# Kernel optimization log

Measured on AMD Instinct MI355X. Metric: run time of the kernel, lower is better.

## Reference

```python
import jax, jax.numpy as jnp
import numpy as np
import math

E = 256; H = 8; MLP = 1024; LAT = 128; TOPK = 32
IH = 4; IDH = 8  # LightningIndexer: num_heads=4, indexer_head_dim=8
B, R, C = 2, 1024, 4


def setup_inputs() -> dict:
    key = jax.random.key(0)
    ks = jax.random.split(key, 12)
    s = 0.02
    def nrm(k, shape, scale=s):
        return jax.random.normal(k, shape, jnp.float32) * scale
    return {
        "src": jax.random.normal(ks[0], (B, R, C, E), jnp.float32),
        "train_test_split_index": 768,
        "fa_in_w": nrm(ks[1], (3 * E, E)), "fa_in_b": jnp.zeros((3 * E,), jnp.float32),
        "fa_out_w": nrm(ks[2], (E, E)), "fa_out_b": jnp.zeros((E,), jnp.float32),
        "norm1_g": jnp.ones((E,), jnp.float32), "norm1_b": jnp.zeros((E,), jnp.float32),
        "idx_q_w": nrm(ks[3], (IH * IDH, E)), "idx_k_w": nrm(ks[4], (IH * IDH, E)),
        "idx_out_w": jax.random.normal(ks[5], (IH,), jnp.float32),
        "mla_q_w": nrm(ks[6], (E, E)), "mla_down_w": nrm(ks[7], (LAT, E)),
        "mla_up_w": nrm(ks[8], (2 * E, LAT)), "mla_out_w": nrm(ks[9], (E, E)),
        "norm2_g": jnp.ones((E,), jnp.float32), "norm2_b": jnp.zeros((E,), jnp.float32),
        "lin1_w": nrm(ks[10], (MLP, E)), "lin1_b": jnp.zeros((MLP,), jnp.float32),
        "lin2_w": nrm(ks[11], (E, MLP)), "lin2_b": jnp.zeros((E,), jnp.float32),
        "norm3_g": jnp.ones((E,), jnp.float32), "norm3_b": jnp.zeros((E,), jnp.float32),
    }


def _ln(x, g, b, eps=1e-5):
    m = x.mean(-1, keepdims=True)
    v = ((x - m) ** 2).mean(-1, keepdims=True)
    return (x - m) * jax.lax.rsqrt(v + eps) * g + b


def _mha(x, in_w, in_b, out_w, out_b):
    # torch nn.MultiheadAttention, batch_first, self-attention
    Bf, S, D = x.shape
    dh = D // H
    qkv = x @ in_w.T + in_b
    q, k, v = jnp.split(qkv, 3, axis=-1)
    q = q.reshape(Bf, S, H, dh); k = k.reshape(Bf, S, H, dh); v = v.reshape(Bf, S, H, dh)
    a = jnp.einsum('bqhd,bkhd->bhqk', q, k) / math.sqrt(dh)
    a = jax.nn.softmax(a, axis=-1)
    o = jnp.einsum('bhqk,bkhd->bqhd', a, v).reshape(Bf, S, D)
    return o @ out_w.T + out_b


def _indexer(xq, xk, qw, kw, ow, top_k):
    # int8-quantized scoring: matmul -> scale -> relu -> head-weighted sum -> topk
    Bf, NQ, _ = xq.shape
    NK = xk.shape[1]
    q = (xq @ qw.T).reshape(Bf, NQ, IH, IDH).transpose(0, 2, 1, 3)  # [B,IH,NQ,IDH]
    k = (xk @ kw.T).reshape(Bf, NK, IH, IDH).transpose(0, 2, 1, 3)
    qs = (jnp.abs(q).max(axis=(2, 3), keepdims=True) + 1e-6) / 127.0
    ks_ = (jnp.abs(k).max(axis=(2, 3), keepdims=True) + 1e-6) / 127.0
    qi = jnp.clip(jnp.round(q / qs), -127, 127)
    ki = jnp.clip(jnp.round(k / ks_), -127, 127)
    scores = jax.nn.relu(jnp.einsum('bhqd,bhkd->bhqk', qi, ki) * (qs * ks_))
    red = jnp.einsum('bhqk,h->bqk', scores, ow)
    _, idx = jax.lax.top_k(red, top_k)
    return idx  # [B, NQ, top_k]


def _mla_sparse(xq, xkv, idx, qw, dw, uw, ow):
    # gather per-query top-k compressed latents, up-project, attend
    Bf, NQ, D = xq.shape
    dh = D // H
    K = idx.shape[2]
    q = (xq @ qw.T).reshape(Bf, NQ, H, dh)
    c = xkv @ dw.T                                    # [B, NKV, LAT]
    c_sel = c[jnp.arange(Bf)[:, None, None], idx]     # [B, NQ, K, LAT]
    kv = (c_sel @ uw.T).reshape(Bf, NQ, K, 2, H, dh)
    k, v = kv[..., 0, :, :], kv[..., 1, :, :]
    score = (q[:, :, None, :, :] * k).sum(-1) / math.sqrt(dh)  # [B,NQ,K,H]
    w = jax.nn.softmax(score, axis=2)
    out = (w[..., None] * v).sum(axis=2).reshape(Bf, NQ, D)
    return out @ ow.T


def reference(src, train_test_split_index, fa_in_w, fa_in_b, fa_out_w, fa_out_b,
              norm1_g, norm1_b, idx_q_w, idx_k_w, idx_out_w,
              mla_q_w, mla_down_w, mla_up_w, mla_out_w,
              norm2_g, norm2_b, lin1_w, lin1_b, lin2_w, lin2_b, norm3_g, norm3_b):
    Bz, Rz, Cz, D = src.shape
    split = int(train_test_split_index)
    # feature attention across columns
    sf = src.reshape(Bz * Rz, Cz, D)
    sf = _mha(sf, fa_in_w, fa_in_b, fa_out_w, fa_out_b) + sf
    src = _ln(sf.reshape(Bz, Rz, Cz, D), norm1_g, norm1_b)
    # row attention with DSA sparse top-k selection
    st = src.transpose(0, 2, 1, 3).reshape(Bz * Cz, Rz, D)
    x_tr, x_te = st[:, :split], st[:, split:]
    k_sel = min(TOPK, split)
    tr_idx = _indexer(x_tr, x_tr, idx_q_w, idx_k_w, idx_out_w, k_sel)
    tr_out = _mla_sparse(x_tr, x_tr, tr_idx, mla_q_w, mla_down_w, mla_up_w, mla_out_w)
    te_idx = _indexer(x_te, x_tr, idx_q_w, idx_k_w, idx_out_w, k_sel)
    te_out = _mla_sparse(x_te, x_tr, te_idx, mla_q_w, mla_down_w, mla_up_w, mla_out_w)
    st = st + jnp.concatenate([tr_out, te_out], axis=1)
    src = st.reshape(Bz, Cz, Rz, D).transpose(0, 2, 1, 3)
    src = _ln(src, norm2_g, norm2_b)
    h = jax.nn.gelu(src @ lin1_w.T + lin1_b, approximate=False)
    src = h @ lin2_w.T + lin2_b + src
    return _ln(src, norm3_g, norm3_b)
```

## Files before the change

### kernel.cpp

```cpp
#include <hip/hip_runtime.h>
#include <hip/hip_bf16.h>
#include <cmath>

#define E_ 256
#define H_ 8
#define DH 32
#define MLPD 1024
#define LATD 128
#define TOPK_ 32
#define BB 2
#define RR 1024
#define CC 4
#define NT 8192
#define BF 8
#define SPLIT 768

using bf16x8 = __attribute__((ext_vector_type(8))) short;
using f32x4v = __attribute__((ext_vector_type(4))) float;

__device__ __forceinline__ unsigned short f2b(float x) {
    __hip_bfloat16 h = __float2bfloat16(x);
    return *reinterpret_cast<unsigned short*>(&h);
}
__device__ __forceinline__ float b2f(unsigned short u) {
    return __uint_as_float(((unsigned)u) << 16);
}

struct ConvArgs {
    const float* s[10];
    unsigned short* d[10];
    int cum[10];
};
__global__ __launch_bounds__(256) void convert_f2b(ConvArgs a, int totq)
{
    int q = blockIdx.x * 256 + threadIdx.x;
    if (q >= totq) return;
    int seg = 0;
    while (q >= a.cum[seg]) seg++;
    int lq = q - (seg ? a.cum[seg - 1] : 0);
    float4 v = ((const float4*)a.s[seg])[lq];
    ushort4 o;
    o.x = f2b(v.x); o.y = f2b(v.y); o.z = f2b(v.z); o.w = f2b(v.w);
    ((ushort4*)a.d[seg])[lq] = o;
}

template<int TM, int TN, int BIAS, int GELU, int RES, int AMAP, int OMAP, int OUTBF>
__global__ __launch_bounds__(256) void gemm_mfma(
    const unsigned short* __restrict__ A, const unsigned short* __restrict__ W,
    const float* __restrict__ bias, const float* __restrict__ res,
    float* __restrict__ Cf, unsigned short* __restrict__ Ch,
    int M, int N, int K)
{
    __shared__ __align__(16) unsigned short As[TM * 40];
    __shared__ __align__(16) unsigned short Bs[TN * 40];
    const int tid = threadIdx.x;
    const int lane = tid & 63, wave = tid >> 6;
    const int wr = wave >> 1, wc = wave & 1;
    const int m0 = blockIdx.y * TM, n0 = blockIdx.x * TN;

    int ra, kqa;
    if constexpr (TM == 128) { ra = tid >> 1; kqa = (tid & 1) * 16; }
    else                     { ra = tid >> 2; kqa = (tid & 3) * 8; }
    int rb, kqb;
    if constexpr (TN == 128) { rb = tid >> 1; kqb = (tid & 1) * 16; }
    else                     { rb = tid >> 2; kqb = (tid & 3) * 8; }

    int am = m0 + ra;
    size_t arow = AMAP ? ((size_t)(am / SPLIT) * RR + (am % SPLIT)) : (size_t)am;
    const unsigned short* Ap = A + arow * (size_t)K + kqa;
    const unsigned short* Bp = W + (size_t)(n0 + rb) * K + kqb;

    constexpr int FM = TM / 32, FN = TN / 32;
    f32x4v acc[FM][FN];
#pragma unroll
    for (int i = 0; i < FM; i++)
#pragma unroll
        for (int j = 0; j < FN; j++) acc[i][j] = (f32x4v){0.f, 0.f, 0.f, 0.f};

    const int kof = (lane >> 4) * 8;
    int arow_lds[FM], brow_lds[FN];
#pragma unroll
    for (int f = 0; f < FM; f++)
        arow_lds[f] = (wr * (TM / 2) + f * 16 + (lane & 15)) * 40 + kof;
#pragma unroll
    for (int f = 0; f < FN; f++)
        brow_lds[f] = (wc * (TN / 2) + f * 16 + (lane & 15)) * 40 + kof;

    for (int k0 = 0; k0 < K; k0 += 32) {
        int4 va0, va1, vb0, vb1;
        va0 = *(const int4*)(Ap + k0);
        if constexpr (TM == 128) va1 = *(const int4*)(Ap + k0 + 8);
        vb0 = *(const int4*)(Bp + k0);
        if constexpr (TN == 128) vb1 = *(const int4*)(Bp + k0 + 8);
        __syncthreads();
        *(int4*)&As[ra * 40 + kqa] = va0;
        if constexpr (TM == 128) *(int4*)&As[ra * 40 + kqa + 8] = va1;
        *(int4*)&Bs[rb * 40 + kqb] = vb0;
        if constexpr (TN == 128) *(int4*)&Bs[rb * 40 + kqb + 8] = vb1;
        __syncthreads();
        bf16x8 af[FM], bfr[FN];
#pragma unroll
        for (int f = 0; f < FM; f++) af[f] = *(const bf16x8*)&As[arow_lds[f]];
#pragma unroll
        for (int f = 0; f < FN; f++) bfr[f] = *(const bf16x8*)&Bs[brow_lds[f]];
#pragma unroll
        for (int fm = 0; fm < FM; fm++)
#pragma unroll
            for (int fn = 0; fn < FN; fn++)
                acc[fm][fn] = __builtin_amdgcn_mfma_f32_16x16x32_bf16(
                    af[fm], bfr[fn], acc[fm][fn], 0, 0, 0);
    }

#pragma unroll
    for (int fm = 0; fm < FM; fm++) {
#pragma unroll
        for (int r = 0; r < 4; r++) {
            int row = m0 + wr * (TM / 2) + fm * 16 + ((lane >> 4) << 2) + r;
            size_t orow;
            if (OMAP) {
                int bc = row >> 10, rr = row & 1023;
                int b = bc >> 2, c = bc & 3;
                orow = ((size_t)(b * RR + rr)) * CC + c;
            } else orow = (size_t)row;
#pragma unroll
            for (int fn = 0; fn < FN; fn++) {
                int col = n0 + wc * (TN / 2) + fn * 16 + (lane & 15);
                float v = acc[fm][fn][r];
                if (BIAS) v += bias[col];
                if (GELU) v = 0.5f * v * (1.0f + erff(v * 0.70710678118654752f));
                if (RES)  v += res[(size_t)row * N + col];
                if (OUTBF) Ch[orow * (size_t)N + col] = f2b(v);
                else       Cf[orow * (size_t)N + col] = v;
            }
        }
    }
}

__global__ __launch_bounds__(256) void fa_attn(const float* __restrict__ qkv,
                                               unsigned short* __restrict__ outb)
{
    int seq = blockIdx.x, tid = threadIdx.x;
    __shared__ float sq[4][E_], sk[4][E_], sv[4][E_];
    __shared__ float ss[H_][4][4];
    __shared__ float sw[H_][4][4];
    const float4* base = (const float4*)(qkv + (size_t)seq * 3072);
#pragma unroll
    for (int p = 0; p < 3; p++) {
        int pos = tid + p * 256;
        float4 v = base[pos];
        int i = pos / 192, c4 = pos % 192;
        if (c4 < 64)       *(float4*)&sq[i][c4 * 4] = v;
        else if (c4 < 128) *(float4*)&sk[i][(c4 - 64) * 4] = v;
        else               *(float4*)&sv[i][(c4 - 128) * 4] = v;
    }
    __syncthreads();
    if (tid < 128) {
        int h = tid >> 4, i = (tid >> 2) & 3, j = tid & 3;
        float s = 0;
        for (int d = 0; d < DH; d++) s += sq[i][h * DH + d] * sk[j][h * DH + d];
        ss[h][i][j] = s * 0.17677669529663688f;
    }
    __syncthreads();
    if (tid < 32) {
        int h = tid >> 2, i = tid & 3;
        float m = ss[h][i][0];
        for (int j = 1; j < 4; j++) m = fmaxf(m, ss[h][i][j]);
        float e[4], sum = 0;
        for (int j = 0; j < 4; j++) { e[j] = expf(ss[h][i][j] - m); sum += e[j]; }
        float inv = 1.0f / sum;
        for (int j = 0; j < 4; j++) sw[h][i][j] = e[j] * inv;
    }
    __syncthreads();
    int e = tid, h = e >> 5;
    for (int i = 0; i < 4; i++) {
        float o = 0;
        for (int j = 0; j < 4; j++) o += sw[h][i][j] * sv[j][e];
        outb[((size_t)(seq * 4 + i)) * E_ + e] = f2b(o);
    }
}

template<int OMAP, int WB>
__global__ __launch_bounds__(256) void ln_k(const float* __restrict__ in,
                                            const float* __restrict__ g,
                                            const float* __restrict__ bta,
                                            float* __restrict__ out,
                                            unsigned short* __restrict__ outh)
{
    int row = blockIdx.x * 4 + (threadIdx.x >> 6);
    int t = threadIdx.x & 63;
    float4 v = ((const float4*)(in + (size_t)row * E_))[t];
    float s = v.x + v.y + v.z + v.w;
#pragma unroll
    for (int o = 32; o >= 1; o >>= 1) s += __shfl_xor(s, o);
    float mean = s * (1.0f / E_);
    float dx0 = v.x - mean, dx1 = v.y - mean, dx2 = v.z - mean, dx3 = v.w - mean;
    float q = dx0 * dx0 + dx1 * dx1 + dx2 * dx2 + dx3 * dx3;
#pragma unroll
    for (int o = 32; o >= 1; o >>= 1) q += __shfl_xor(q, o);
    float inv = rsqrtf(q * (1.0f / E_) + 1e-5f);
    size_t orow;
    if (OMAP == 1) {
        int b = row >> 12, r = (row >> 2) & 1023, c = row & 3;
        orow = ((size_t)(b * CC + c)) * RR + r;
    } else orow = (size_t)row;
    int c0 = t * 4;
    float4 o;
    o.x = dx0 * inv * g[c0 + 0] + bta[c0 + 0];
    o.y = dx1 * inv * g[c0 + 1] + bta[c0 + 1];
    o.z = dx2 * inv * g[c0 + 2] + bta[c0 + 2];
    o.w = dx3 * inv * g[c0 + 3] + bta[c0 + 3];
    ((float4*)(out + orow * E_))[t] = o;
    if (WB) {
        ushort4 oh; oh.x = f2b(o.x); oh.y = f2b(o.y); oh.z = f2b(o.z); oh.w = f2b(o.w);
        ((ushort4*)(outh + orow * E_))[t] = oh;
    }
}

__global__ __launch_bounds__(256) void idx_scales(const float* __restrict__ qk32,
                                                  float* __restrict__ scl)
{
    int id = blockIdx.x;
    int type = id / 32, bf = (id % 32) >> 2, h = id & 3;
    int cofs = (type == 2) ? 32 : 0;
    int r0 = (type == 1) ? SPLIT : 0;
    int r1 = (type == 1) ? RR : SPLIT;
    float m = 0;
    for (int r = r0 + (int)threadIdx.x; r < r1; r += 256) {
        const float* p = qk32 + ((size_t)(bf * RR + r)) * 64 + cofs + h * 8;
        for (int dd = 0; dd < 8; dd++) m = fmaxf(m, fabsf(p[dd]));
    }
#pragma unroll
    for (int o = 32; o >= 1; o >>= 1) m = fmaxf(m, __shfl_xor(m, o));
    __shared__ float red[4];
    if ((threadIdx.x & 63) == 0) red[threadIdx.x >> 6] = m;
    __syncthreads();
    if (threadIdx.x == 0) {
        m = fmaxf(fmaxf(red[0], red[1]), fmaxf(red[2], red[3]));
        scl[id] = (m + 1e-6f) / 127.0f;
    }
}

__global__ __launch_bounds__(256) void idx_quantk(const float* __restrict__ qk32,
                                                  const float* __restrict__ scl,
                                                  signed char* __restrict__ ki8)
{
    int gi = blockIdx.x * 256 + threadIdx.x;
    int bf = gi / (SPLIT * 32);
    int rem = gi % (SPLIT * 32);
    int r = rem >> 5, d = rem & 31, h = d >> 3;
    float ks = scl[64 + bf * 4 + h];
    float v = qk32[((size_t)(bf * RR + r)) * 64 + 32 + d];
    float qq = fminf(fmaxf(rintf(v / ks), -127.f), 127.f);
    ki8[gi] = (signed char)qq;
}

__global__ __launch_bounds__(256) void idx_score_topk(const float* __restrict__ qk32,
                                                      const signed char* __restrict__ ki8,
                                                      const float* __restrict__ scl,
                                                      const float* __restrict__ ow,
                                                      int* __restrict__ idx_out)
{
    int bid = blockIdx.x, tid = threadIdx.x;
    int bf = bid >> 10, qr = bid & 1023;
    int sel = (qr < SPLIT) ? 0 : 32;
    __shared__ float qi[32];
    __shared__ float fac[4];
    __shared__ unsigned keyhi[SPLIT];
    __shared__ __align__(16) unsigned long long cand[SPLIT];
    __shared__ int hist[256], hist2[256], Sarr[256];
    __shared__ int bsel1, bsel2, ccnt;

    hist[tid] = 0; hist2[tid] = 0;
    if (tid == 0) ccnt = 0;
    if (tid < 32) {
        int h = tid >> 3;
        float qs = scl[sel + bf * 4 + h];
        float v = qk32[(size_t)bid * 64 + tid];
        qi[tid] = fminf(fmaxf(rintf(v / qs), -127.f), 127.f);
    }
    if (tid < 4) {
        float qs = scl[sel + bf * 4 + tid];
        float ks = scl[64 + bf * 4 + tid];
        fac[tid] = __fmul_rn(qs, ks);
    }
    __syncthreads();
    float ow0 = ow[0], ow1 = ow[1], ow2 = ow[2], ow3 = ow[3];
    for (int k = tid; k < SPLIT; k += 256) {
        const int4* kp4 = (const int4*)(ki8 + ((size_t)(bf * SPLIT + k)) * 32);
        int4 w0 = kp4[0], w1 = kp4[1];
        int wd[8] = {w0.x, w0.y, w0.z, w0.w, w1.x, w1.y, w1.z, w1.w};
        float owv[4] = {ow0, ow1, ow2, ow3};
        float r = 0;
#pragma unroll
        for (int h = 0; h < 4; h++) {
            float dot = 0.f;
#pragma unroll
            for (int b = 0; b < 2; b++) {
                unsigned int w = (unsigned int)wd[h * 2 + b];
#pragma unroll
                for (int by = 0; by < 4; by++) {
                    float kv = (float)((signed char)(w >> (8 * by)));
                    dot = fmaf(qi[h * 8 + b * 4 + by], kv, dot);
                }
            }
            float sc = fmaxf(__fmul_rn(dot, fac[h]), 0.f);
            r = __fadd_rn(r, __fmul_rn(sc, owv[h]));
        }
        unsigned int bitsv = __float_as_uint(r);
        unsigned int mono = (bitsv & 0x80000000u) ? ~bitsv : (bitsv | 0x80000000u);
        if (mono == 0x7FFFFFFFu) mono = 0x80000000u;
        keyhi[k] = mono;
        atomicAdd(&hist[mono >> 24], 1);
    }
    __syncthreads();
    if (tid < 64) {
        int4 h4 = *(const int4*)&hist[tid * 4];
        int local = h4.x + h4.y + h4.z + h4.w;
        int s = local;
#pragma unroll
        for (int o = 1; o < 64; o <<= 1) {
            int x = __shfl_down(s, o);
            if (tid + o < 64) s += x;
        }
        int sufE = s - local;
        Sarr[tid * 4 + 0] = sufE + h4.y + h4.z + h4.w;
        Sarr[tid * 4 + 1] = sufE + h4.z + h4.w;
        Sarr[tid * 4 + 2] = sufE + h4.w;
        Sarr[tid * 4 + 3] = sufE;
    }
    __syncthreads();
    if (Sarr[tid] < TOPK_ && Sarr[tid] + hist[tid] >= TOPK_) bsel1 = tid;
    __syncthreads();
    const int b1 = bsel1;
    const int S1 = Sarr[b1];
    for (int k = tid; k < SPLIT; k += 256) {
        unsigned mono = keyhi[k];
        if ((int)(mono >> 24) == b1) atomicAdd(&hist2[(mono >> 16) & 255], 1);
    }
    __syncthreads();
    if (tid < 64) {
        int4 h4 = *(const int4*)&hist2[tid * 4];
        int local = h4.x + h4.y + h4.z + h4.w;
        int s = local;
#pragma unroll
        for (int o = 1; o < 64; o <<= 1) {
            int x = __shfl_down(s, o);
            if (tid + o < 64) s += x;
        }
        int sufE = s - local;
        Sarr[tid * 4 + 0] = sufE + h4.y + h4.z + h4.w;
        Sarr[tid * 4 + 1] = sufE + h4.z + h4.w;
        Sarr[tid * 4 + 2] = sufE + h4.w;
        Sarr[tid * 4 + 3] = sufE;
    }
    __syncthreads();
    if (S1 + Sarr[tid] < TOPK_ && S1 + Sarr[tid] + hist2[tid] >= TOPK_) bsel2 = tid;
    __syncthreads();
    const int b2 = bsel2;
    for (int k = tid; k < SPLIT; k += 256) {
        unsigned mono = keyhi[k];
        int hi = mono >> 24, mid = (mono >> 16) & 255;
        if (hi > b1 || (hi == b1 && mid >= b2)) {
            int s = atomicAdd(&ccnt, 1);
            cand[s] = ((unsigned long long)mono << 10) | (unsigned)(1023 - k);
        }
    }
    __syncthreads();
    const int n = ccnt;
    for (int ci = tid; ci < n; ci += 256) {
        unsigned long long mine = cand[ci];
        int r = 0;
        for (int j = 0; j < n; j++) r += (cand[j] > mine);
        if (r < TOPK_)
            idx_out[(size_t)bid * TOPK_ + r] = 1023 - (int)(mine & 1023ull);
    }
}

__global__ __launch_bounds__(256) void mla_g(const float* __restrict__ qb,
                                             const float* __restrict__ uw,
                                             unsigned short* __restrict__ G16)
{
    int qt = blockIdx.x, h = blockIdx.y, tid = threadIdx.x;
    __shared__ float Qs[64][33];
    __shared__ float Us[32][132];
    {
        int r = tid >> 2, c0 = (tid & 3) * 8;
        const float* srcp = qb + ((size_t)(qt * 64 + r)) * E_ + h * DH + c0;
        float4 a = ((const float4*)srcp)[0];
        float4 b = ((const float4*)srcp)[1];
        Qs[r][c0 + 0] = a.x; Qs[r][c0 + 1] = a.y; Qs[r][c0 + 2] = a.z; Qs[r][c0 + 3] = a.w;
        Qs[r][c0 + 4] = b.x; Qs[r][c0 + 5] = b.y; Qs[r][c0 + 6] = b.z; Qs[r][c0 + 7] = b.w;
    }
    {
        int d = tid >> 3, l0 = (tid & 7) * 16;
        const float* srcp = uw + (size_t)(h * DH + d) * LATD + l0;
#pragma unroll
        for (int ii = 0; ii < 4; ii++) {
            float4 v = ((const float4*)srcp)[ii];
            *(float4*)&Us[d][l0 + ii * 4] = v;
        }
    }
    __syncthreads();
    int rg = tid >> 5, l = (tid & 31) * 4;
    float acc[8][4];
#pragma unroll
    for (int i = 0; i < 8; i++)
#pragma unroll
        for (int j = 0; j < 4; j++) acc[i][j] = 0.f;
    for (int d = 0; d < DH; d++) {
        float4 u = *(const float4*)&Us[d][l];
#pragma unroll
        for (int i = 0; i < 8; i++) {
            float qv = Qs[rg * 8 + i][d];
            acc[i][0] += qv * u.x; acc[i][1] += qv * u.y;
            acc[i][2] += qv * u.z; acc[i][3] += qv * u.w;
        }
    }
#pragma unroll
    for (int i = 0; i < 8; i++) {
        ushort4 o;
        o.x = f2b(acc[i][0]); o.y = f2b(acc[i][1]);
        o.z = f2b(acc[i][2]); o.w = f2b(acc[i][3]);
        *(ushort4*)(G16 + ((size_t)(qt * 64 + rg * 8 + i)) * 1024 + h * 128 + l) = o;
    }
}

__global__ __launch_bounds__(64) void mla_attn(const unsigned short* __restrict__ G16,
                                               const unsigned short* __restrict__ cb16,
                                               const int* __restrict__ idxb,
                                               unsigned short* __restrict__ Mo16)
{
    const int bid = blockIdx.x, l = threadIdx.x;
    const int bf = bid >> 10;
    __shared__ __align__(16) unsigned short ct[128][40];
    __shared__ __align__(16) unsigned short wT[16][40];
    __shared__ int sidx[32];
    if (l < 32) sidx[l] = idxb[(size_t)bid * 32 + l];

    const int n16 = l & 15, g = l >> 4;

    {
        int j = l >> 1, c0 = (l & 1) * 64;
        const unsigned short* crow = cb16 + ((size_t)(bf * SPLIT + sidx[j])) * 128 + c0;
#pragma unroll
        for (int e = 0; e < 8; e++) {
            uint4 v = *(const uint4*)(crow + e * 8);
            unsigned short tmp[8];
            *(uint4*)tmp = v;
#pragma unroll
            for (int t = 0; t < 8; t++) ct[c0 + e * 8 + t][j] = tmp[t];
        }
    }

    const unsigned short* Ab = G16 + (size_t)bid * 1024 + (size_t)(l & 7) * 128 + g * 8;
    const int j0 = sidx[n16], j1 = sidx[16 + n16];
    const unsigned short* B0 = cb16 + ((size_t)(bf * SPLIT + j0)) * 128 + g * 8;
    const unsigned short* B1 = cb16 + ((size_t)(bf * SPLIT + j1)) * 128 + g * 8;
    f32x4v s0 = {0.f, 0.f, 0.f, 0.f}, s1 = {0.f, 0.f, 0.f, 0.f};
#pragma unroll
    for (int c = 0; c < 4; c++) {
        bf16x8 a  = *(const bf16x8*)(Ab + c * 32);
        bf16x8 b0 = *(const bf16x8*)(B0 + c * 32);
        bf16x8 b1 = *(const bf16x8*)(B1 + c * 32);
        s0 = __builtin_amdgcn_mfma_f32_16x16x32_bf16(a, b0, s0, 0, 0, 0);
        s1 = __builtin_amdgcn_mfma_f32_16x16x32_bf16(a, b1, s1, 0, 0, 0);
    }

    const float scale = 0.17677669529663688f;
#pragma unroll
    for (int r = 0; r < 4; r++) {
        float a0 = s0[r] * scale, a1 = s1[r] * scale;
        float mx = fmaxf(a0, a1);
#pragma unroll
        for (int o = 1; o < 16; o <<= 1) mx = fmaxf(mx, __shfl_xor(mx, o));
        float e0 = expf(a0 - mx), e1 = expf(a1 - mx);
        float sm = e0 + e1;
#pragma unroll
        for (int o = 1; o < 16; o <<= 1) sm += __shfl_xor(sm, o);
        float inv = 1.0f / sm;
        wT[g * 4 + r][n16]      = f2b(e0 * inv);
        wT[g * 4 + r][16 + n16] = f2b(e1 * inv);
    }

    bf16x8 aw = *(const bf16x8*)&wT[n16][g * 8];
#pragma unroll
    for (int t = 0; t < 8; t++) {
        bf16x8 bc = *(const bf16x8*)&ct[t * 16 + n16][g * 8];
        f32x4v m = {0.f, 0.f, 0.f, 0.f};
        m = __builtin_amdgcn_mfma_f32_16x16x32_bf16(aw, bc, m, 0, 0, 0);
        if (g < 2) {
#pragma unroll
            for (int r = 0; r < 4; r++)
                Mo16[(size_t)bid * 1024 + (size_t)(g * 4 + r) * 128 + t * 16 + n16] = f2b(m[r]);
        }
    }
}

__global__ __launch_bounds__(256) void mla_out(const unsigned short* __restrict__ Mo16,
                                               const float* __restrict__ uw,
                                               unsigned short* __restrict__ ob)
{
    int qt = blockIdx.x, h = blockIdx.y, tid = threadIdx.x;
    __shared__ float Ms[64][132];
    __shared__ float Us[32][129];
    {
        int r = tid >> 2, l0 = (tid & 3) * 32;
        const unsigned short* srcp = Mo16 + ((size_t)(qt * 64 + r)) * 1024 + h * 128 + l0;
#pragma unroll
        for (int ii = 0; ii < 4; ii++) {
            uint4 v = ((const uint4*)srcp)[ii];
            unsigned short u[8];
            *(uint4*)u = v;
#pragma unroll
            for (int t = 0; t < 8; t++) Ms[r][l0 + ii * 8 + t] = b2f(u[t]);
        }
    }
    {
        int d = tid >> 3, l0 = (tid & 7) * 16;
        const float* srcp = uw + (size_t)(256 + h * DH + d) * LATD + l0;
#pragma unroll
        for (int ii = 0; ii < 4; ii++) {
            float4 v = ((const float4*)srcp)[ii];
            Us[d][l0 + ii * 4 + 0] = v.x; Us[d][l0 + ii * 4 + 1] = v.y;
            Us[d][l0 + ii * 4 + 2] = v.z; Us[d][l0 + ii * 4 + 3] = v.w;
        }
    }
    __syncthreads();
    int d = tid & 31, rg = tid >> 5;
    float acc[8] = {0, 0, 0, 0, 0, 0, 0, 0};
    for (int ll = 0; ll < 128; ll++) {
        float u = Us[d][ll];
#pragma unroll
        for (int i = 0; i < 8; i++) acc[i] += Ms[rg * 8 + i][ll] * u;
    }
#pragma unroll
    for (int i = 0; i < 8; i++)
        ob[((size_t)(qt * 64 + rg * 8 + i)) * E_ + h * DH + d] = f2b(acc[i]);
}

extern "C" void kernel_launch(void* const* d_in, const int* in_sizes, int n_in,
                              void* d_out, int out_size, void* d_ws, size_t ws_size,
                              hipStream_t stream)
{
    (void)in_sizes; (void)n_in; (void)out_size; (void)ws_size;
    const float* src      = (const float*)d_in[0];
    const float* fa_in_w  = (const float*)d_in[2];
    const float* fa_in_b  = (const float*)d_in[3];
    const float* fa_out_w = (const float*)d_in[4];
    const float* fa_out_b = (const float*)d_in[5];
    const float* n1g = (const float*)d_in[6];
    const float* n1b = (const float*)d_in[7];
    const float* iqw = (const float*)d_in[8];
    const float* ikw = (const float*)d_in[9];
    const float* iow = (const float*)d_in[10];
    const float* mqw = (const float*)d_in[11];
    const float* mdw = (const float*)d_in[12];
    const float* muw = (const float*)d_in[13];
    const float* mow = (const float*)d_in[14];
    const float* n2g = (const float*)d_in[15];
    const float* n2b = (const float*)d_in[16];
    const float* l1w = (const float*)d_in[17];
    const float* l1b = (const float*)d_in[18];
    const float* l2w = (const float*)d_in[19];
    const float* l2b = (const float*)d_in[20];
    const float* n3g = (const float*)d_in[21];
    const float* n3b = (const float*)d_in[22];

    float* ws = (float*)d_ws;
    size_t off = 0;
    auto alloc = [&](size_t n) { float* p = ws + off; off += (n + 3) & ~(size_t)3; return p; };

    float* bigA = alloc((size_t)NT * 1024);
    float* Mh   = alloc((size_t)NT * 1024);
    float* tbuf = alloc((size_t)NT * E_);
    float* stb  = alloc((size_t)NT * E_);
    float* cbws = alloc((size_t)BF * SPLIT * LATD / 2 + 16);
    unsigned short* actBF1 = (unsigned short*)alloc((size_t)NT * E_ / 2);
    unsigned short* actBF2 = (unsigned short*)alloc((size_t)NT * E_ / 2);
    float* qk32 = alloc((size_t)NT * 64);
    float* scl = alloc(128);
    int*   idxb = (int*)alloc((size_t)NT * 32);
    signed char* ki8 = (signed char*)alloc((size_t)NT * 32 / 4);
    unsigned short* w16 = (unsigned short*)alloc(950272 / 2 + 8);
    unsigned short* wqk16 = (unsigned short*)alloc(16384 / 2 + 8);

    unsigned short* fa_in_w16  = w16;
    unsigned short* fa_out_w16 = fa_in_w16 + 196608;
    unsigned short* mqw16      = fa_out_w16 + 65536;
    unsigned short* mdw16      = mqw16 + 65536;
    unsigned short* mow16      = mdw16 + 32768;
    unsigned short* l1w16      = mow16 + 65536;
    unsigned short* l2w16      = l1w16 + 262144;

    float* qkv = bigA;
    unsigned short* G16 = (unsigned short*)bigA;
    float* x2  = bigA;
    unsigned short* Mo16 = (unsigned short*)Mh;
    unsigned short* h116 = (unsigned short*)Mh;
    float* qb = tbuf;
    unsigned short* cb16 = (unsigned short*)cbws;
    unsigned short* src16  = actBF1;
    unsigned short* abuf16 = actBF1;
    unsigned short* stb16  = actBF1;
    unsigned short* ob16   = actBF2;
    unsigned short* x216   = actBF2;

    ConvArgs ca;
    const float* segs[10] = {src, fa_in_w, fa_out_w, mqw, mdw, mow, l1w, l2w, iqw, ikw};
    unsigned short* segd[10] = {src16, fa_in_w16, fa_out_w16, mqw16, mdw16, mow16, l1w16, l2w16,
                                wqk16, wqk16 + 8192};
    int segn[10] = {NT * E_, 196608, 65536, 65536, 32768, 65536, 262144, 262144, 8192, 8192};
    int cum = 0;
    for (int i = 0; i < 10; i++) { ca.s[i] = segs[i]; ca.d[i] = segd[i]; cum += segn[i] / 4; ca.cum[i] = cum; }
    int totq = cum;
    convert_f2b<<<(totq + 255) / 256, 256, 0, stream>>>(ca, totq);

    dim3 blk(256);
    gemm_mfma<128,128,1,0,0,0,0,0><<<dim3(6,64), blk, 0, stream>>>(src16, fa_in_w16, fa_in_b, nullptr, qkv, nullptr, NT, 768, 256);
    fa_attn<<<2048, blk, 0, stream>>>(qkv, abuf16);
    gemm_mfma<128,64,1,0,1,0,0,0><<<dim3(4,64), blk, 0, stream>>>(abuf16, fa_out_w16, fa_out_b, src, tbuf, nullptr, NT, 256, 256);
    ln_k<1,1><<<NT/4, blk, 0, stream>>>(tbuf, n1g, n1b, stb, stb16);
    gemm_mfma<128,64,0,0,0,0,0,0><<<dim3(1,64), blk, 0, stream>>>(stb16, wqk16, nullptr, nullptr, qk32, nullptr, NT, 64, 256);
    idx_scales<<<96, blk, 0, stream>>>(qk32, scl);
    idx_quantk<<<(BF * SPLIT * 32) / 256, blk, 0, stream>>>(qk32, scl, ki8);
    idx_score_topk<<<NT, blk, 0, stream>>>(qk32, ki8, scl, iow, idxb);
    gemm_mfma<64,64,0,0,0,1,0,1><<<dim3(2,96), blk, 0, stream>>>(stb16, mdw16, nullptr, nullptr, nullptr, cb16, BF * SPLIT, 128, 256);
    gemm_mfma<128,64,0,0,0,0,0,0><<<dim3(4,64), blk, 0, stream>>>(stb16, mqw16, nullptr, nullptr, qb, nullptr, NT, 256, 256);
    mla_g<<<dim3(128,8), blk, 0, stream>>>(qb, muw, G16);
    mla_attn<<<NT, dim3(64), 0, stream>>>(G16, cb16, idxb, Mo16);
    mla_out<<<dim3(128,8), blk, 0, stream>>>(Mo16, muw, ob16);
    gemm_mfma<128,64,0,0,1,0,1,0><<<dim3(4,64), blk, 0, stream>>>(ob16, mow16, nullptr, stb, tbuf, nullptr, NT, 256, 256);
    ln_k<0,1><<<NT/4, blk, 0, stream>>>(tbuf, n2g, n2b, x2, x216);
    gemm_mfma<128,128,1,1,0,0,0,1><<<dim3(8,64), blk, 0, stream>>>(x216, l1w16, l1b, nullptr, nullptr, h116, NT, MLPD, 256);
    gemm_mfma<128,64,1,0,1,0,0,0><<<dim3(4,64), blk, 0, stream>>>(h116, l2w16, l2b, x2, tbuf, nullptr, NT, 256, MLPD);
    ln_k<0,0><<<NT/4, blk, 0, stream>>>(tbuf, n3g, n3b, (float*)d_out, nullptr);
}
```

Measured before the change: 309.6 us.

## Fold MLA query/up/out projections into precomputed weights and merge indexer kernels

Precomputes W2 = U_k^T·Wq and W3 = Wo·U_v per head in a new weight-prep kernel. This replaces the q-projection GEMM, the mla_g kernel, the mla_out kernel and the output GEMM with two MFMA GEMMs (K=256→N=1024 and K=1024→N=256). The QKV projection now writes bf16 instead of fp32 to halve traffic into fa_attn. idx_scales and idx_quantk are merged into one kernel, and mla_attn packs four queries per 256-thread block. The trade-off is extra rounding from the bf16 products of the folded weights and a per-call weight-fold kernel.

```diff
diff --git a/kernel.cpp b/kernel.cpp
--- a/kernel.cpp
+++ b/kernel.cpp
@@ -27,9 +27,9 @@
 }
 
 struct ConvArgs {
-    const float* s[10];
-    unsigned short* d[10];
-    int cum[10];
+    const float* s[8];
+    unsigned short* d[8];
+    int cum[8];
 };
 __global__ __launch_bounds__(256) void convert_f2b(ConvArgs a, int totq)
 {
@@ -42,6 +42,33 @@
     ushort4 o;
     o.x = f2b(v.x); o.y = f2b(v.y); o.z = f2b(v.z); o.w = f2b(v.w);
     ((ushort4*)a.d[seg])[lq] = o;
+}
+
+__global__ __launch_bounds__(256) void make_w2w3(const float* __restrict__ mqw,
+                                                 const float* __restrict__ muw,
+                                                 const float* __restrict__ mow,
+                                                 unsigned short* __restrict__ W2,
+                                                 unsigned short* __restrict__ W3)
+{
+    int b = blockIdx.x, t = threadIdx.x;
+    if (b < 1024) {
+        int h = b >> 7, l = b & 127;
+        float s2 = 0;
+#pragma unroll 8
+        for (int d = 0; d < 32; d++)
+            s2 += muw[(size_t)(h * 32 + d) * 128 + l] * mqw[(size_t)(h * 32 + d) * 256 + t];
+        W2[(size_t)b * 256 + t] = f2b(s2);
+    } else {
+        int e = b - 1024;
+        for (int tt = t; tt < 1024; tt += 256) {
+            int h = tt >> 7, l = tt & 127;
+            float s3 = 0;
+#pragma unroll 8
+            for (int d = 0; d < 32; d++)
+                s3 += muw[(size_t)(256 + h * 32 + d) * 128 + l] * mow[(size_t)e * 256 + h * 32 + d];
+            W3[(size_t)e * 1024 + tt] = f2b(s3);
+        }
+    }
 }
 
 template<int TM, int TN, int BIAS, int GELU, int RES, int AMAP, int OMAP, int OUTBF>
@@ -136,22 +163,27 @@
     }
 }
 
-__global__ __launch_bounds__(256) void fa_attn(const float* __restrict__ qkv,
+__global__ __launch_bounds__(256) void fa_attn(const unsigned short* __restrict__ qkv16,
                                                unsigned short* __restrict__ outb)
 {
     int seq = blockIdx.x, tid = threadIdx.x;
     __shared__ float sq[4][E_], sk[4][E_], sv[4][E_];
     __shared__ float ss[H_][4][4];
     __shared__ float sw[H_][4][4];
-    const float4* base = (const float4*)(qkv + (size_t)seq * 3072);
-#pragma unroll
-    for (int p = 0; p < 3; p++) {
+    const uint4* base = (const uint4*)(qkv16 + (size_t)seq * 3072);
+#pragma unroll
+    for (int p = 0; p < 2; p++) {
         int pos = tid + p * 256;
-        float4 v = base[pos];
-        int i = pos / 192, c4 = pos % 192;
-        if (c4 < 64)       *(float4*)&sq[i][c4 * 4] = v;
-        else if (c4 < 128) *(float4*)&sk[i][(c4 - 64) * 4] = v;
-        else               *(float4*)&sv[i][(c4 - 128) * 4] = v;
+        if (pos < 384) {
+            uint4 v = base[pos];
+            unsigned short u[8];
+            *(uint4*)u = v;
+            int flat = pos * 8;
+            int i = flat / 768, c = flat % 768;
+            float* dst = (c < 256) ? &sq[i][c] : (c < 512) ? &sk[i][c - 256] : &sv[i][c - 512];
+#pragma unroll
+            for (int t = 0; t < 8; t++) dst[t] = b2f(u[t]);
+        }
     }
     __syncthreads();
     if (tid < 128) {
@@ -216,8 +248,9 @@
     }
 }
 
-__global__ __launch_bounds__(256) void idx_scales(const float* __restrict__ qk32,
-                                                  float* __restrict__ scl)
+__global__ __launch_bounds__(256) void idx_scales_quant(const float* __restrict__ qk32,
+                                                        float* __restrict__ scl,
+                                                        signed char* __restrict__ ki8)
 {
     int id = blockIdx.x;
     int type = id / 32, bf = (id % 32) >> 2, h = id & 3;
@@ -232,26 +265,26 @@
 #pragma unroll
     for (int o = 32; o >= 1; o >>= 1) m = fmaxf(m, __shfl_xor(m, o));
     __shared__ float red[4];
+    __shared__ float sscl;
     if ((threadIdx.x & 63) == 0) red[threadIdx.x >> 6] = m;
     __syncthreads();
     if (threadIdx.x == 0) {
         m = fmaxf(fmaxf(red[0], red[1]), fmaxf(red[2], red[3]));
-        scl[id] = (m + 1e-6f) / 127.0f;
-    }
-}
-
-__global__ __launch_bounds__(256) void idx_quantk(const float* __restrict__ qk32,
-                                                  const float* __restrict__ scl,
-                                                  signed char* __restrict__ ki8)
-{
-    int gi = blockIdx.x * 256 + threadIdx.x;
-    int bf = gi / (SPLIT * 32);
-    int rem = gi % (SPLIT * 32);
-    int r = rem >> 5, d = rem & 31, h = d >> 3;
-    float ks = scl[64 + bf * 4 + h];
-    float v = qk32[((size_t)(bf * RR + r)) * 64 + 32 + d];
-    float qq = fminf(fmaxf(rintf(v / ks), -127.f), 127.f);
-    ki8[gi] = (signed char)qq;
+        float sc = (m + 1e-6f) / 127.0f;
+        scl[id] = sc;
+        sscl = sc;
+    }
+    __syncthreads();
+    if (type == 2) {
+        float ks = sscl;
+        for (int r = threadIdx.x; r < SPLIT; r += 256) {
+            const float* p = qk32 + ((size_t)(bf * RR + r)) * 64 + 32 + h * 8;
+            signed char* o = ki8 + ((size_t)(bf * SPLIT + r)) * 32 + h * 8;
+#pragma unroll
+            for (int dd = 0; dd < 8; dd++)
+                o[dd] = (signed char)fminf(fmaxf(rintf(p[dd] / ks), -127.f), 127.f);
+        }
+    }
 }
 
 __global__ __launch_bounds__(256) void idx_score_topk(const float* __restrict__ qk32,
@@ -376,84 +409,36 @@
     }
 }
 
-__global__ __launch_bounds__(256) void mla_g(const float* __restrict__ qb,
-                                             const float* __restrict__ uw,
-                                             unsigned short* __restrict__ G16)
-{
-    int qt = blockIdx.x, h = blockIdx.y, tid = threadIdx.x;
-    __shared__ float Qs[64][33];
-    __shared__ float Us[32][132];
-    {
-        int r = tid >> 2, c0 = (tid & 3) * 8;
-        const float* srcp = qb + ((size_t)(qt * 64 + r)) * E_ + h * DH + c0;
-        float4 a = ((const float4*)srcp)[0];
-        float4 b = ((const float4*)srcp)[1];
-        Qs[r][c0 + 0] = a.x; Qs[r][c0 + 1] = a.y; Qs[r][c0 + 2] = a.z; Qs[r][c0 + 3] = a.w;
-        Qs[r][c0 + 4] = b.x; Qs[r][c0 + 5] = b.y; Qs[r][c0 + 6] = b.z; Qs[r][c0 + 7] = b.w;
-    }
-    {
-        int d = tid >> 3, l0 = (tid & 7) * 16;
-        const float* srcp = uw + (size_t)(h * DH + d) * LATD + l0;
-#pragma unroll
-        for (int ii = 0; ii < 4; ii++) {
-            float4 v = ((const float4*)srcp)[ii];
-            *(float4*)&Us[d][l0 + ii * 4] = v;
-        }
-    }
-    __syncthreads();
-    int rg = tid >> 5, l = (tid & 31) * 4;
-    float acc[8][4];
-#pragma unroll
-    for (int i = 0; i < 8; i++)
-#pragma unroll
-        for (int j = 0; j < 4; j++) acc[i][j] = 0.f;
-    for (int d = 0; d < DH; d++) {
-        float4 u = *(const float4*)&Us[d][l];
-#pragma unroll
-        for (int i = 0; i < 8; i++) {
-            float qv = Qs[rg * 8 + i][d];
-            acc[i][0] += qv * u.x; acc[i][1] += qv * u.y;
-            acc[i][2] += qv * u.z; acc[i][3] += qv * u.w;
-        }
-    }
-#pragma unroll
-    for (int i = 0; i < 8; i++) {
-        ushort4 o;
-        o.x = f2b(acc[i][0]); o.y = f2b(acc[i][1]);
-        o.z = f2b(acc[i][2]); o.w = f2b(acc[i][3]);
-        *(ushort4*)(G16 + ((size_t)(qt * 64 + rg * 8 + i)) * 1024 + h * 128 + l) = o;
-    }
-}
-
-__global__ __launch_bounds__(64) void mla_attn(const unsigned short* __restrict__ G16,
-                                               const unsigned short* __restrict__ cb16,
-                                               const int* __restrict__ idxb,
-                                               unsigned short* __restrict__ Mo16)
-{
-    const int bid = blockIdx.x, l = threadIdx.x;
+__global__ __launch_bounds__(256) void mla_attn(const unsigned short* __restrict__ G16,
+                                                const unsigned short* __restrict__ cb16,
+                                                const int* __restrict__ idxb,
+                                                unsigned short* __restrict__ Mo16)
+{
+    const int w = threadIdx.x >> 6, l = threadIdx.x & 63;
+    const int bid = blockIdx.x * 4 + w;
     const int bf = bid >> 10;
-    __shared__ __align__(16) unsigned short ct[128][40];
-    __shared__ __align__(16) unsigned short wT[16][40];
-    __shared__ int sidx[32];
-    if (l < 32) sidx[l] = idxb[(size_t)bid * 32 + l];
+    __shared__ __align__(16) unsigned short ct[4][128][40];
+    __shared__ __align__(16) unsigned short wT[4][16][40];
+    __shared__ int sidx[4][32];
+    if (l < 32) sidx[w][l] = idxb[(size_t)bid * 32 + l];
 
     const int n16 = l & 15, g = l >> 4;
 
     {
         int j = l >> 1, c0 = (l & 1) * 64;
-        const unsigned short* crow = cb16 + ((size_t)(bf * SPLIT + sidx[j])) * 128 + c0;
+        const unsigned short* crow = cb16 + ((size_t)(bf * SPLIT + sidx[w][j])) * 128 + c0;
 #pragma unroll
         for (int e = 0; e < 8; e++) {
             uint4 v = *(const uint4*)(crow + e * 8);
             unsigned short tmp[8];
             *(uint4*)tmp = v;
 #pragma unroll
-            for (int t = 0; t < 8; t++) ct[c0 + e * 8 + t][j] = tmp[t];
+            for (int t = 0; t < 8; t++) ct[w][c0 + e * 8 + t][j] = tmp[t];
         }
     }
 
     const unsigned short* Ab = G16 + (size_t)bid * 1024 + (size_t)(l & 7) * 128 + g * 8;
-    const int j0 = sidx[n16], j1 = sidx[16 + n16];
+    const int j0 = sidx[w][n16], j1 = sidx[w][16 + n16];
     const unsigned short* B0 = cb16 + ((size_t)(bf * SPLIT + j0)) * 128 + g * 8;
     const unsigned short* B1 = cb16 + ((size_t)(bf * SPLIT + j1)) * 128 + g * 8;
     f32x4v s0 = {0.f, 0.f, 0.f, 0.f}, s1 = {0.f, 0.f, 0.f, 0.f};
@@ -478,14 +463,14 @@
 #pragma unroll
         for (int o = 1; o < 16; o <<= 1) sm += __shfl_xor(sm, o);
         float inv = 1.0f / sm;
-        wT[g * 4 + r][n16]      = f2b(e0 * inv);
-        wT[g * 4 + r][16 + n16] = f2b(e1 * inv);
-    }
-
-    bf16x8 aw = *(const bf16x8*)&wT[n16][g * 8];
+        wT[w][g * 4 + r][n16]      = f2b(e0 * inv);
+        wT[w][g * 4 + r][16 + n16] = f2b(e1 * inv);
+    }
+
+    bf16x8 aw = *(const bf16x8*)&wT[w][n16][g * 8];
 #pragma unroll
     for (int t = 0; t < 8; t++) {
-        bf16x8 bc = *(const bf16x8*)&ct[t * 16 + n16][g * 8];
+        bf16x8 bc = *(const bf16x8*)&ct[w][t * 16 + n16][g * 8];
         f32x4v m = {0.f, 0.f, 0.f, 0.f};
         m = __builtin_amdgcn_mfma_f32_16x16x32_bf16(aw, bc, m, 0, 0, 0);
         if (g < 2) {
@@ -494,48 +479,6 @@
                 Mo16[(size_t)bid * 1024 + (size_t)(g * 4 + r) * 128 + t * 16 + n16] = f2b(m[r]);
         }
     }
-}
-
-__global__ __launch_bounds__(256) void mla_out(const unsigned short* __restrict__ Mo16,
-                                               const float* __restrict__ uw,
-                                               unsigned short* __restrict__ ob)
-{
-    int qt = blockIdx.x, h = blockIdx.y, tid = threadIdx.x;
-    __shared__ float Ms[64][132];
-    __shared__ float Us[32][129];
-    {
-        int r = tid >> 2, l0 = (tid & 3) * 32;
-        const unsigned short* srcp = Mo16 + ((size_t)(qt * 64 + r)) * 1024 + h * 128 + l0;
-#pragma unroll
-        for (int ii = 0; ii < 4; ii++) {
-            uint4 v = ((const uint4*)srcp)[ii];
-            unsigned short u[8];
-            *(uint4*)u = v;
-#pragma unroll
-            for (int t = 0; t < 8; t++) Ms[r][l0 + ii * 8 + t] = b2f(u[t]);
-        }
-    }
-    {
-        int d = tid >> 3, l0 = (tid & 7) * 16;
-        const float* srcp = uw + (size_t)(256 + h * DH + d) * LATD + l0;
-#pragma unroll
-        for (int ii = 0; ii < 4; ii++) {
-            float4 v = ((const float4*)srcp)[ii];
-            Us[d][l0 + ii * 4 + 0] = v.x; Us[d][l0 + ii * 4 + 1] = v.y;
-            Us[d][l0 + ii * 4 + 2] = v.z; Us[d][l0 + ii * 4 + 3] = v.w;
-        }
-    }
-    __syncthreads();
-    int d = tid & 31, rg = tid >> 5;
-    float acc[8] = {0, 0, 0, 0, 0, 0, 0, 0};
-    for (int ll = 0; ll < 128; ll++) {
-        float u = Us[d][ll];
-#pragma unroll
-        for (int i = 0; i < 8; i++) acc[i] += Ms[rg * 8 + i][ll] * u;
-    }
-#pragma unroll
-    for (int i = 0; i < 8; i++)
-        ob[((size_t)(qt * 64 + rg * 8 + i)) * E_ + h * DH + d] = f2b(acc[i]);
 }
 
 extern "C" void kernel_launch(void* const* d_in, const int* in_sizes, int n_in,
@@ -581,55 +524,51 @@
     float* scl = alloc(128);
     int*   idxb = (int*)alloc((size_t)NT * 32);
     signed char* ki8 = (signed char*)alloc((size_t)NT * 32 / 4);
-    unsigned short* w16 = (unsigned short*)alloc(950272 / 2 + 8);
+    unsigned short* w16 = (unsigned short*)alloc(819200 / 2 + 16);
     unsigned short* wqk16 = (unsigned short*)alloc(16384 / 2 + 8);
+    unsigned short* W2_16 = (unsigned short*)alloc(262144 / 2 + 8);
+    unsigned short* W3_16 = (unsigned short*)alloc(262144 / 2 + 8);
 
     unsigned short* fa_in_w16  = w16;
     unsigned short* fa_out_w16 = fa_in_w16 + 196608;
-    unsigned short* mqw16      = fa_out_w16 + 65536;
-    unsigned short* mdw16      = mqw16 + 65536;
-    unsigned short* mow16      = mdw16 + 32768;
-    unsigned short* l1w16      = mow16 + 65536;
+    unsigned short* mdw16      = fa_out_w16 + 65536;
+    unsigned short* l1w16      = mdw16 + 32768;
     unsigned short* l2w16      = l1w16 + 262144;
 
-    float* qkv = bigA;
+    unsigned short* qkv16 = (unsigned short*)bigA;
     unsigned short* G16 = (unsigned short*)bigA;
     float* x2  = bigA;
     unsigned short* Mo16 = (unsigned short*)Mh;
     unsigned short* h116 = (unsigned short*)Mh;
-    float* qb = tbuf;
     unsigned short* cb16 = (unsigned short*)cbws;
     unsigned short* src16  = actBF1;
     unsigned short* abuf16 = actBF1;
     unsigned short* stb16  = actBF1;
-    unsigned short* ob16   = actBF2;
     unsigned short* x216   = actBF2;
 
     ConvArgs ca;
-    const float* segs[10] = {src, fa_in_w, fa_out_w, mqw, mdw, mow, l1w, l2w, iqw, ikw};
-    unsigned short* segd[10] = {src16, fa_in_w16, fa_out_w16, mqw16, mdw16, mow16, l1w16, l2w16,
-                                wqk16, wqk16 + 8192};
-    int segn[10] = {NT * E_, 196608, 65536, 65536, 32768, 65536, 262144, 262144, 8192, 8192};
+    const float* segs[8] = {src, fa_in_w, fa_out_w, mdw, l1w, l2w, iqw, ikw};
+    unsigned short* segd[8] = {src16, fa_in_w16, fa_out_w16, mdw16, l1w16, l2w16,
+                               wqk16, wqk16 + 8192};
+    int segn[8] = {NT * E_, 196608, 65536, 32768, 262144, 262144, 8192, 8192};
     int cum = 0;
-    for (int i = 0; i < 10; i++) { ca.s[i] = segs[i]; ca.d[i] = segd[i]; cum += segn[i] / 4; ca.cum[i] = cum; }
+    for (int i = 0; i < 8; i++) { ca.s[i] = segs[i]; ca.d[i] = segd[i]; cum += segn[i] / 4; ca.cum[i] = cum; }
     int totq = cum;
     convert_f2b<<<(totq + 255) / 256, 256, 0, stream>>>(ca, totq);
+    make_w2w3<<<1280, 256, 0, stream>>>(mqw, muw, mow, W2_16, W3_16);
 
     dim3 blk(256);
-    gemm_mfma<128,128,1,0,0,0,0,0><<<dim3(6,64), blk, 0, stream>>>(src16, fa_in_w16, fa_in_b, nullptr, qkv, nullptr, NT, 768, 256);
-    fa_attn<<<2048, blk, 0, stream>>>(qkv, abuf16);
+    gemm_mfma<128,128,1,0,0,0,0,1><<<dim3(6,64), blk, 0, stream>>>(src16, fa_in_w16, fa_in_b, nullptr, nullptr, qkv16, NT, 768, 256);
+    fa_attn<<<2048, blk, 0, stream>>>(qkv16, abuf16);
     gemm_mfma<128,64,1,0,1,0,0,0><<<dim3(4,64), blk, 0, stream>>>(abuf16, fa_out_w16, fa_out_b, src, tbuf, nullptr, NT, 256, 256);
     ln_k<1,1><<<NT/4, blk, 0, stream>>>(tbuf, n1g, n1b, stb, stb16);
     gemm_mfma<128,64,0,0,0,0,0,0><<<dim3(1,64), blk, 0, stream>>>(stb16, wqk16, nullptr, nullptr, qk32, nullptr, NT, 64, 256);
-    idx_scales<<<96, blk, 0, stream>>>(qk32, scl);
-    idx_quantk<<<(BF * SPLIT * 32) / 256, blk, 0, stream>>>(qk32, scl, ki8);
+    idx_scales_quant<<<96, blk, 0, stream>>>(qk32, scl, ki8);
     idx_score_topk<<<NT, blk, 0, stream>>>(qk32, ki8, scl, iow, idxb);
     gemm_mfma<64,64,0,0,0,1,0,1><<<dim3(2,96), blk, 0, stream>>>(stb16, mdw16, nullptr, nullptr, nullptr, cb16, BF * SPLIT, 128, 256);
-    gemm_mfma<128,64,0,0,0,0,0,0><<<dim3(4,64), blk, 0, stream>>>(stb16, mqw16, nullptr, nullptr, qb, nullptr, NT, 256, 256);
-    mla_g<<<dim3(128,8), blk, 0, stream>>>(qb, muw, G16);
-    mla_attn<<<NT, dim3(64), 0, stream>>>(G16, cb16, idxb, Mo16);
-    mla_out<<<dim3(128,8), blk, 0, stream>>>(Mo16, muw, ob16);
-    gemm_mfma<128,64,0,0,1,0,1,0><<<dim3(4,64), blk, 0, stream>>>(ob16, mow16, nullptr, stb, tbuf, nullptr, NT, 256, 256);
+    gemm_mfma<128,128,0,0,0,0,0,1><<<dim3(8,64), blk, 0, stream>>>(stb16, W2_16, nullptr, nullptr, nullptr, G16, NT, 1024, 256);
+    mla_attn<<<NT/4, blk, 0, stream>>>(G16, cb16, idxb, Mo16);
+    gemm_mfma<128,128,0,0,1,0,1,0><<<dim3(2,64), blk, 0, stream>>>(Mo16, W3_16, nullptr, stb, tbuf, nullptr, NT, 256, 1024);
     ln_k<0,1><<<NT/4, blk, 0, stream>>>(tbuf, n2g, n2b, x2, x216);
     gemm_mfma<128,128,1,1,0,0,0,1><<<dim3(8,64), blk, 0, stream>>>(x216, l1w16, l1b, nullptr, nullptr, h116, NT, MLPD, 256);
     gemm_mfma<128,64,1,0,1,0,0,0><<<dim3(4,64), blk, 0, stream>>>(h116, l2w16, l2b, x2, tbuf, nullptr, NT, 256, MLPD);
```

Measured after the change: 319.3 us. 1.03x slower.
